# Kernel optimization log

Hardware: AMD Instinct MI355X
Metric: run time of the kernel (lower is better)

## Reference

```python
import jax, jax.numpy as jnp
import numpy as np

B, F, V, D = 4096, 24, 1000, 32
RED = 8            # max(1, F // 3) SENet bottleneck
COMB = 2 * F * D   # 1536
EPS = 1e-5


def setup_inputs() -> dict:
    key = jax.random.key(0)
    ks = jax.random.split(key, 12)
    return {
        "x": jax.random.randint(ks[0], (B, F), 0, V),
        "emb_tables": jax.random.normal(ks[1], (F, V, D), jnp.float32) * 0.05,
        "lin_tables": jax.random.normal(ks[2], (F, V), jnp.float32) * 0.05,
        "bias": jnp.zeros((1,), jnp.float32),
        "se_w1": jax.random.normal(ks[3], (RED, F), jnp.float32) * 0.2,
        "se_w2": jax.random.normal(ks[4], (F, RED), jnp.float32) * 0.2,
        "bil_W": jax.random.normal(ks[5], (F, F, D, D), jnp.float32) * (1.0 / np.sqrt(D)),
        "w0": jax.random.normal(ks[6], (COMB, 1024), jnp.float32) * 0.02,
        "b0": jnp.zeros((1024,), jnp.float32),
        "g0": jnp.ones((1024,), jnp.float32),
        "be0": jnp.zeros((1024,), jnp.float32),
        "w1": jax.random.normal(ks[7], (1024, 512), jnp.float32) * 0.02,
        "b1": jnp.zeros((512,), jnp.float32),
        "g1": jnp.ones((512,), jnp.float32),
        "be1": jnp.zeros((512,), jnp.float32),
        "w2": jax.random.normal(ks[8], (512, 1), jnp.float32) * 0.02,
        "b2": jnp.zeros((1,), jnp.float32),
    }


def _bilinear_field_interaction(e, W):
    # e: [B,F,D], W: [F,F,D,D]
    # out[b,i,k] = e[b,i,k] * sum_{j != i} (W[i,j] @ e[b,j])[k]
    t = jnp.einsum('ijkl,bjl->bijk', W, e)          # [B,F,F,D]
    mask = 1.0 - jnp.eye(F, dtype=e.dtype)          # zero the i==j terms
    s = jnp.einsum('bijk,ij->bik', t, mask)         # [B,F,D]
    return e * s


def _senet(e, w1, w2):
    Z = e.mean(axis=2)                              # [B,F] squeeze
    A = jax.nn.sigmoid(jax.nn.relu(Z @ w1.T) @ w2.T)  # [B,F]
    return e * A[:, :, None]


def _bn_train(h, g, b):
    m = h.mean(axis=0)
    v = h.var(axis=0)  # biased, matches torch BN normalization
    return g * (h - m) * jax.lax.rsqrt(v + EPS) + b


def reference(x, emb_tables, lin_tables, bias, se_w1, se_w2, bil_W,
              w0, b0, g0, be0, w1, b1, g1, be1, w2, b2):
    fidx = jnp.arange(F)[None, :]                   # [1,F]
    emb = emb_tables[fidx, x]                       # [B,F,D]
    lin = lin_tables[fidx, x].sum(axis=1)           # [B] first-order term

    se_emb = _senet(emb, se_w1, se_w2)
    p = _bilinear_field_interaction(emb, bil_W)     # [B,F,D]
    q = _bilinear_field_interaction(se_emb, bil_W)  # [B,F,D]
    combined = jnp.concatenate(
        [p.reshape(B, F * D), q.reshape(B, F * D)], axis=1)  # [B,2FD]

    h = jax.nn.relu(_bn_train(combined @ w0 + b0, g0, be0))
    h = jax.nn.relu(_bn_train(h @ w1 + b1, g1, be1))
    mlp_out = (h @ w2 + b2)[:, 0]                   # [B]

    logit = lin + bias[0] + mlp_out
    return jax.nn.sigmoid(logit)                    # [B]
```

## Files before the change

kernel.cpp:

```cpp
#include <hip/hip_runtime.h>

#define B_SZ 4096
#define F_SZ 24
#define V_SZ 1000
#define D_SZ 32
#define RED  8
#define FD   768
#define COMB 1536
#define H0   1024
#define H1   512
#define EPS  1e-5f

typedef __bf16 bf16x8 __attribute__((ext_vector_type(8)));
typedef float  f32x4  __attribute__((ext_vector_type(4)));
typedef const __attribute__((address_space(1))) unsigned int* gptr_t;
typedef       __attribute__((address_space(3))) unsigned int* lptr_t;

__device__ __forceinline__ float bf2f(unsigned short u) {
    union { unsigned int i; float f; } v; v.i = ((unsigned int)u) << 16; return v.f;
}
__device__ __forceinline__ unsigned short f2bf(float f) {
    union { float f; unsigned int i; } v; v.f = f;
    unsigned int u = v.i;
    return (unsigned short)((u + 0x7FFFu + ((u >> 16) & 1u)) >> 16);
}
__device__ __forceinline__ unsigned int pack2(float a, float b) {
    return (unsigned int)f2bf(a) | ((unsigned int)f2bf(b) << 16);
}

__global__ __launch_bounds__(256) void prep_gather(
        const int* __restrict__ x, const float* __restrict__ emb,
        const float* __restrict__ lint, const float* __restrict__ sw1,
        const float* __restrict__ sw2, const float* __restrict__ bw,
        const float* __restrict__ w0, const float* __restrict__ w1,
        unsigned short* __restrict__ Xbf, unsigned short* __restrict__ Wt,
        unsigned short* __restrict__ w0t, unsigned short* __restrict__ w1t,
        float* __restrict__ lin, float* __restrict__ sums) {
    int bid = blockIdx.x;
    int tid = threadIdx.x;
    if (bid < 1024) {
        int w = tid >> 6, lane = tid & 63;
        int b = bid * 4 + w;
        __shared__ int   xi[4][F_SZ];
        __shared__ float e[4][F_SZ][D_SZ];
        __shared__ float Z[4][F_SZ];
        __shared__ float r1[4][RED];
        __shared__ float Afac[4][F_SZ];
        if (lane < F_SZ) xi[w][lane] = x[b * F_SZ + lane];
        __syncthreads();
        #pragma unroll
        for (int it = 0; it < 3; it++) {
            int idx = it * 64 + lane;
            int f = idx >> 3, k4 = (idx & 7) * 4;
            float4 v = *(const float4*)&emb[((size_t)f * V_SZ + xi[w][f]) * D_SZ + k4];
            *(float4*)&e[w][f][k4] = v;
        }
        __syncthreads();
        if (lane < F_SZ) {
            float s = 0.f;
            #pragma unroll
            for (int k = 0; k < D_SZ; k++) s += e[w][lane][k];
            Z[w][lane] = s * (1.f / D_SZ);
        }
        __syncthreads();
        if (lane < RED) {
            float s = 0.f;
            #pragma unroll
            for (int f = 0; f < F_SZ; f++) s += Z[w][f] * sw1[lane * F_SZ + f];
            r1[w][lane] = fmaxf(s, 0.f);
        }
        __syncthreads();
        if (lane < F_SZ) {
            float s = 0.f;
            #pragma unroll
            for (int r = 0; r < RED; r++) s += r1[w][r] * sw2[lane * RED + r];
            Afac[w][lane] = 1.f / (1.f + expf(-s));
        }
        __syncthreads();
        #pragma unroll
        for (int it = 0; it < 3; it++) {
            int idx = it * 64 + lane;
            int f = idx >> 3, k4 = (idx & 7) * 4;
            const float* p = &e[w][f][k4];
            uint2 u, us;
            u.x = pack2(p[0], p[1]); u.y = pack2(p[2], p[3]);
            float a = Afac[w][f];
            us.x = pack2(p[0] * a, p[1] * a); us.y = pack2(p[2] * a, p[3] * a);
            *(uint2*)&Xbf[(size_t)b * FD + idx * 4] = u;
            *(uint2*)&Xbf[(size_t)(B_SZ + b) * FD + idx * 4] = us;
        }
        float lv = (lane < F_SZ) ? lint[lane * V_SZ + xi[w][lane]] : 0.f;
        #pragma unroll
        for (int off = 32; off > 0; off >>= 1) lv += __shfl_down(lv, off);
        if (lane == 0) lin[b] = lv;
    } else if (bid < 3328) {
        int o = (bid - 1024) * 256 + tid;
        int ik = o / FD, jl = o - ik * FD;
        int i = ik >> 5, k = ik & 31, j = jl >> 5, l = jl & 31;
        Wt[o] = (i == j) ? (unsigned short)0
                         : f2bf(bw[(((size_t)i * F_SZ + j) * D_SZ + k) * D_SZ + l]);
    } else if (bid < 5376) {
        __shared__ float tile[32][33];
        const float* in; unsigned short* out; int K, N, bx, by;
        if (bid < 4864) { int t = bid - 3328; in = w0; out = w0t; K = COMB; N = H0; bx = t & 31; by = t >> 5; }
        else            { int t = bid - 4864; in = w1; out = w1t; K = H0;   N = H1; bx = t & 15; by = t >> 4; }
        int tx = tid & 31, ty = tid >> 5;
        int n0 = bx * 32, k0 = by * 32;
        #pragma unroll
        for (int r = 0; r < 32; r += 8)
            tile[ty + r][tx] = in[(size_t)(k0 + ty + r) * N + n0 + tx];
        __syncthreads();
        #pragma unroll
        for (int r = 0; r < 32; r += 8)
            out[(size_t)(n0 + ty + r) * K + k0 + tx] = f2bf(tile[tx][ty + r]);
    } else {
        int o = (bid - 5376) * 256 + tid;
        sums[o] = 0.f;
    }
}

template<int MODE, int K, int N, int TM, int TN, int GX, int GY>
__global__ __launch_bounds__(256) void mfma_gemm(
        const unsigned short* __restrict__ A,
        const unsigned short* __restrict__ Bt,
        const float* __restrict__ bias,
        const unsigned short* __restrict__ Xbf,
        unsigned short* __restrict__ Obf,
        float* __restrict__ sum, float* __restrict__ sumsq,
        const float* __restrict__ psum, const float* __restrict__ psumsq,
        const float* __restrict__ g, const float* __restrict__ be) {
    constexpr int MI = TM / 32, NI = TN / 32;
    __shared__ unsigned short Abuf[TM * 32];
    __shared__ unsigned short Bbuf[TN * 32];
    __shared__ float sc_s[MODE == 2 ? K : 1];
    __shared__ float sh_s[MODE == 2 ? K : 1];
    const int tid  = threadIdx.x;
    const int lane = tid & 63, wv = tid >> 6;
    const int wm = (wv >> 1) * (TM / 2), wn = (wv & 1) * (TN / 2);
    const int fr = lane & 15, kq = lane >> 4;
    const int bid = blockIdx.x;
    const int xcd = bid & 7, slot = bid >> 3;
    const int rowb = xcd * (GY / 8) + slot / GX;
    const int colb = slot % GX;
    const int bm = rowb * TM, bn = colb * TN;
    const int srow = tid >> 2;
    const int skc  = (tid & 3) * 8;

    if (MODE == 2) {
        #pragma unroll
        for (int q = 0; q < K / 256; q++) {
            int c = q * 256 + tid;
            float m = psum[c] * (1.f / B_SZ);
            float var = psumsq[c] * (1.f / B_SZ) - m * m;
            float rstd = rsqrtf(var + EPS);
            float sc = g[c] * rstd;
            sc_s[c] = sc;
            sh_s[c] = be[c] - m * sc;
        }
        __syncthreads();
    }

    f32x4 acc[MI][NI];
    #pragma unroll
    for (int i = 0; i < MI; i++)
        #pragma unroll
        for (int j = 0; j < NI; j++) {
            f32x4 z = {0.f, 0.f, 0.f, 0.f};
            acc[i][j] = z;
        }

    for (int k0 = 0; k0 < K; k0 += 32) {
        if (MODE == 2) {
            uint4 hv = *(const uint4*)&A[(size_t)(bm + srow) * K + k0 + skc];
            unsigned int uu[4] = {hv.x, hv.y, hv.z, hv.w};
            unsigned int oo[4];
            #pragma unroll
            for (int q = 0; q < 4; q++) {
                int c = k0 + skc + 2 * q;
                float v0 = bf2f((unsigned short)(uu[q] & 0xFFFF)) * sc_s[c] + sh_s[c];
                float v1 = bf2f((unsigned short)(uu[q] >> 16)) * sc_s[c + 1] + sh_s[c + 1];
                oo[q] = pack2(fmaxf(v0, 0.f), fmaxf(v1, 0.f));
            }
            uint4 ov; ov.x = oo[0]; ov.y = oo[1]; ov.z = oo[2]; ov.w = oo[3];
            *(uint4*)&Abuf[srow * 32 + skc] = ov;
        } else {
            #pragma unroll
            for (int c = 0; c < TM / 64; c++) {
                const unsigned short* ga = A + (size_t)(bm + c * 64 + srow) * K + k0 + skc;
                char* la = (char*)Abuf + c * 4096 + wv * 1024;
                __builtin_amdgcn_global_load_lds((gptr_t)ga, (lptr_t)la, 16, 0, 0);
            }
        }
        #pragma unroll
        for (int c = 0; c < TN / 64; c++) {
            const unsigned short* gb = Bt + (size_t)(bn + c * 64 + srow) * K + k0 + skc;
            char* lb = (char*)Bbuf + c * 4096 + wv * 1024;
            __builtin_amdgcn_global_load_lds((gptr_t)gb, (lptr_t)lb, 16, 0, 0);
        }
        __syncthreads();
        bf16x8 af[MI], bfv[NI];
        #pragma unroll
        for (int mi = 0; mi < MI; mi++)
            af[mi] = *(const bf16x8*)&Abuf[(wm + mi * 16 + fr) * 32 + kq * 8];
        #pragma unroll
        for (int ni = 0; ni < NI; ni++)
            bfv[ni] = *(const bf16x8*)&Bbuf[(wn + ni * 16 + fr) * 32 + kq * 8];
        #pragma unroll
        for (int mi = 0; mi < MI; mi++)
            #pragma unroll
            for (int ni = 0; ni < NI; ni++)
                acc[mi][ni] = __builtin_amdgcn_mfma_f32_16x16x32_bf16(
                    af[mi], bfv[ni], acc[mi][ni], 0, 0, 0);
        __syncthreads();
    }

    if (MODE == 0) {
        #pragma unroll
        for (int mi = 0; mi < MI; mi++)
            #pragma unroll
            for (int ni = 0; ni < NI; ni++) {
                int col = bn + wn + ni * 16 + fr;
                #pragma unroll
                for (int r = 0; r < 4; r++) {
                    int row = bm + wm + mi * 16 + kq * 4 + r;
                    float xv = bf2f(Xbf[(size_t)row * FD + col]);
                    float cv = xv * acc[mi][ni][r];
                    size_t off = (row < B_SZ)
                        ? ((size_t)row * COMB + col)
                        : ((size_t)(row - B_SZ) * COMB + FD + col);
                    Obf[off] = f2bf(cv);
                }
            }
    } else {
        #pragma unroll
        for (int ni = 0; ni < NI; ni++) {
            int col = bn + wn + ni * 16 + fr;
            float bv = bias[col];
            float s = 0.f, ss = 0.f;
            #pragma unroll
            for (int mi = 0; mi < MI; mi++)
                #pragma unroll
                for (int r = 0; r < 4; r++) {
                    int row = bm + wm + mi * 16 + kq * 4 + r;
                    float v = acc[mi][ni][r] + bv;
                    Obf[(size_t)row * N + col] = f2bf(v);
                    s += v; ss += v * v;
                }
            s  += __shfl_xor(s, 16);  s  += __shfl_xor(s, 32);
            ss += __shfl_xor(ss, 16); ss += __shfl_xor(ss, 32);
            if (kq == 0) {
                atomicAdd(&sum[col], s);
                atomicAdd(&sumsq[col], ss);
            }
        }
    }
}

__global__ __launch_bounds__(256) void final_k(const unsigned short* __restrict__ h1,
        const float* __restrict__ sum, const float* __restrict__ sumsq,
        const float* __restrict__ g, const float* __restrict__ be,
        const float* __restrict__ w2, const float* __restrict__ b2,
        const float* __restrict__ lin, const float* __restrict__ bias,
        float* __restrict__ out) {
    __shared__ float sc_s[H1], sh_s[H1], w2_s[H1];
    int t = threadIdx.x;
    int wv = t >> 6, lane = t & 63;
    #pragma unroll
    for (int q = 0; q < 2; q++) {
        int c = q * 256 + t;
        float m = sum[c] * (1.f / B_SZ);
        float var = sumsq[c] * (1.f / B_SZ) - m * m;
        float rstd = rsqrtf(var + EPS);
        float sc = g[c] * rstd;
        sc_s[c] = sc;
        sh_s[c] = be[c] - m * sc;
        w2_s[c] = w2[c];
    }
    __syncthreads();
    int r0 = blockIdx.x * 16;
    #pragma unroll
    for (int i = 0; i < 4; i++) {
        int row = r0 + wv * 4 + i;
        int c0 = lane * 8;
        uint4 hv = *(const uint4*)&h1[(size_t)row * H1 + c0];
        unsigned int uu[4] = {hv.x, hv.y, hv.z, hv.w};
        float acc = 0.f;
        #pragma unroll
        for (int q = 0; q < 4; q++) {
            int c = c0 + 2 * q;
            float v0 = bf2f((unsigned short)(uu[q] & 0xFFFF)) * sc_s[c] + sh_s[c];
            float v1 = bf2f((unsigned short)(uu[q] >> 16)) * sc_s[c + 1] + sh_s[c + 1];
            acc += fmaxf(v0, 0.f) * w2_s[c] + fmaxf(v1, 0.f) * w2_s[c + 1];
        }
        #pragma unroll
        for (int off = 32; off > 0; off >>= 1) acc += __shfl_down(acc, off);
        if (lane == 0) {
            float logit = lin[row] + bias[0] + acc + b2[0];
            out[row] = 1.f / (1.f + expf(-logit));
        }
    }
}

extern "C" void kernel_launch(void* const* d_in, const int* in_sizes, int n_in,
                              void* d_out, int out_size, void* d_ws, size_t ws_size,
                              hipStream_t stream) {
    const int*   x    = (const int*)d_in[0];
    const float* emb  = (const float*)d_in[1];
    const float* lint = (const float*)d_in[2];
    const float* bias = (const float*)d_in[3];
    const float* sw1  = (const float*)d_in[4];
    const float* sw2  = (const float*)d_in[5];
    const float* bw   = (const float*)d_in[6];
    const float* w0   = (const float*)d_in[7];
    const float* b0   = (const float*)d_in[8];
    const float* g0   = (const float*)d_in[9];
    const float* be0  = (const float*)d_in[10];
    const float* w1   = (const float*)d_in[11];
    const float* b1   = (const float*)d_in[12];
    const float* g1   = (const float*)d_in[13];
    const float* be1  = (const float*)d_in[14];
    const float* w2   = (const float*)d_in[15];
    const float* b2   = (const float*)d_in[16];
    float* out = (float*)d_out;

    char* p = (char*)d_ws;
    auto alloc = [&](size_t bytes) { char* r = p; p += (bytes + 255) & ~(size_t)255; return r; };

    unsigned short* Xbf  = (unsigned short*)alloc((size_t)2 * B_SZ * FD * 2);
    unsigned short* Wt   = (unsigned short*)alloc((size_t)FD * FD * 2);
    unsigned short* w0t  = (unsigned short*)alloc((size_t)H0 * COMB * 2);
    unsigned short* w1t  = (unsigned short*)alloc((size_t)H1 * H0 * 2);
    unsigned short* Cbf  = (unsigned short*)alloc((size_t)B_SZ * COMB * 2);
    unsigned short* h0bf = (unsigned short*)alloc((size_t)B_SZ * H0 * 2);
    unsigned short* h1bf = (unsigned short*)alloc((size_t)B_SZ * H1 * 2);
    float* lin = (float*)alloc(B_SZ * 4);
    float* sums = (float*)alloc((2 * H0 + 2 * H1) * 4);
    float* sum0 = sums, *sumsq0 = sums + H0, *sum1 = sums + 2 * H0, *sumsq1 = sums + 2 * H0 + H1;

    prep_gather<<<5388, 256, 0, stream>>>(x, emb, lint, sw1, sw2, bw, w0, w1,
                                          Xbf, Wt, w0t, w1t, lin, sums);

    mfma_gemm<0, FD, FD, 128, 64, 12, 64><<<768, 256, 0, stream>>>(
        Xbf, Wt, nullptr, Xbf, Cbf, nullptr, nullptr, nullptr, nullptr, nullptr, nullptr);
    mfma_gemm<1, COMB, H0, 128, 64, 16, 32><<<512, 256, 0, stream>>>(
        Cbf, w0t, b0, nullptr, h0bf, sum0, sumsq0, nullptr, nullptr, nullptr, nullptr);
    mfma_gemm<2, H0, H1, 64, 64, 8, 64><<<512, 256, 0, stream>>>(
        h0bf, w1t, b1, nullptr, h1bf, sum1, sumsq1, sum0, sumsq0, g0, be0);
    final_k<<<B_SZ / 16, 256, 0, stream>>>(h1bf, sum1, sumsq1, g1, be1,
                                           w2, b2, lin, bias, out);
}
```

Before: 177.3 us.

## Double K-step per barrier and stage GEMM epilogue through LDS for vector stores

The MFMA GEMM main loop now loads two 32-wide K slices per iteration, which halves the number of __syncthreads barriers. In the BN-fused mode it also prefetches the next A slice into registers before the MFMAs run. The epilogue writes the accumulators into a padded LDS tile and then emits 16-byte bf16 stores, with the X-multiply applied during that pass, instead of scattered 2-byte stores. The cost is more LDS use per block, which may lower occupancy. The store pass assumes a 64-column tile per 32-row pass.

```diff
diff --git a/kernel.cpp b/kernel.cpp
--- a/kernel.cpp
+++ b/kernel.cpp
@@ -130,8 +130,14 @@
         const float* __restrict__ psum, const float* __restrict__ psumsq,
         const float* __restrict__ g, const float* __restrict__ be) {
     constexpr int MI = TM / 32, NI = TN / 32;
-    __shared__ unsigned short Abuf[TM * 32];
-    __shared__ unsigned short Bbuf[TN * 32];
+    constexpr int CLD = TN + 4;
+    constexpr int STAGE = (TM + TN) * 128;
+    constexpr int CST   = TM * CLD * 4;
+    constexpr int SMEM  = STAGE > CST ? STAGE : CST;
+    __shared__ __align__(16) char smem[SMEM];
+    unsigned short* Abuf = (unsigned short*)smem;
+    unsigned short* Bbuf = (unsigned short*)(smem + TM * 128);
+    float* Cst = (float*)smem;
     __shared__ float sc_s[MODE == 2 ? K : 1];
     __shared__ float sh_s[MODE == 2 ? K : 1];
     const int tid  = threadIdx.x;
@@ -169,69 +175,73 @@
             acc[i][j] = z;
         }
 
-    for (int k0 = 0; k0 < K; k0 += 32) {
+    uint4 hvA[2];
+    if (MODE == 2) {
+        #pragma unroll
+        for (int s = 0; s < 2; s++)
+            hvA[s] = *(const uint4*)&A[(size_t)(bm + srow) * K + 32 * s + skc];
+    }
+
+    for (int k0 = 0; k0 < K; k0 += 64) {
         if (MODE == 2) {
-            uint4 hv = *(const uint4*)&A[(size_t)(bm + srow) * K + k0 + skc];
-            unsigned int uu[4] = {hv.x, hv.y, hv.z, hv.w};
-            unsigned int oo[4];
-            #pragma unroll
-            for (int q = 0; q < 4; q++) {
-                int c = k0 + skc + 2 * q;
-                float v0 = bf2f((unsigned short)(uu[q] & 0xFFFF)) * sc_s[c] + sh_s[c];
-                float v1 = bf2f((unsigned short)(uu[q] >> 16)) * sc_s[c + 1] + sh_s[c + 1];
-                oo[q] = pack2(fmaxf(v0, 0.f), fmaxf(v1, 0.f));
+            #pragma unroll
+            for (int s = 0; s < 2; s++) {
+                unsigned int uu[4] = {hvA[s].x, hvA[s].y, hvA[s].z, hvA[s].w};
+                unsigned int oo[4];
+                #pragma unroll
+                for (int q = 0; q < 4; q++) {
+                    int c = k0 + 32 * s + skc + 2 * q;
+                    float v0 = bf2f((unsigned short)(uu[q] & 0xFFFF)) * sc_s[c] + sh_s[c];
+                    float v1 = bf2f((unsigned short)(uu[q] >> 16)) * sc_s[c + 1] + sh_s[c + 1];
+                    oo[q] = pack2(fmaxf(v0, 0.f), fmaxf(v1, 0.f));
+                }
+                uint4 ov; ov.x = oo[0]; ov.y = oo[1]; ov.z = oo[2]; ov.w = oo[3];
+                *(uint4*)&Abuf[s * TM * 32 + srow * 32 + skc] = ov;
             }
-            uint4 ov; ov.x = oo[0]; ov.y = oo[1]; ov.z = oo[2]; ov.w = oo[3];
-            *(uint4*)&Abuf[srow * 32 + skc] = ov;
+            if (k0 + 64 < K) {
+                #pragma unroll
+                for (int s = 0; s < 2; s++)
+                    hvA[s] = *(const uint4*)&A[(size_t)(bm + srow) * K + k0 + 64 + 32 * s + skc];
+            }
         } else {
             #pragma unroll
-            for (int c = 0; c < TM / 64; c++) {
-                const unsigned short* ga = A + (size_t)(bm + c * 64 + srow) * K + k0 + skc;
-                char* la = (char*)Abuf + c * 4096 + wv * 1024;
-                __builtin_amdgcn_global_load_lds((gptr_t)ga, (lptr_t)la, 16, 0, 0);
+            for (int s = 0; s < 2; s++)
+                #pragma unroll
+                for (int c = 0; c < TM / 64; c++) {
+                    const unsigned short* ga = A + (size_t)(bm + c * 64 + srow) * K + k0 + 32 * s + skc;
+                    char* la = smem + s * TM * 64 + c * 4096 + wv * 1024;
+                    __builtin_amdgcn_global_load_lds((gptr_t)ga, (lptr_t)la, 16, 0, 0);
+                }
+        }
+        #pragma unroll
+        for (int s = 0; s < 2; s++)
+            #pragma unroll
+            for (int c = 0; c < TN / 64; c++) {
+                const unsigned short* gb = Bt + (size_t)(bn + c * 64 + srow) * K + k0 + 32 * s + skc;
+                char* lb = smem + TM * 128 + s * TN * 64 + c * 4096 + wv * 1024;
+                __builtin_amdgcn_global_load_lds((gptr_t)gb, (lptr_t)lb, 16, 0, 0);
             }
-        }
-        #pragma unroll
-        for (int c = 0; c < TN / 64; c++) {
-            const unsigned short* gb = Bt + (size_t)(bn + c * 64 + srow) * K + k0 + skc;
-            char* lb = (char*)Bbuf + c * 4096 + wv * 1024;
-            __builtin_amdgcn_global_load_lds((gptr_t)gb, (lptr_t)lb, 16, 0, 0);
-        }
-        __syncthreads();
-        bf16x8 af[MI], bfv[NI];
-        #pragma unroll
-        for (int mi = 0; mi < MI; mi++)
-            af[mi] = *(const bf16x8*)&Abuf[(wm + mi * 16 + fr) * 32 + kq * 8];
-        #pragma unroll
-        for (int ni = 0; ni < NI; ni++)
-            bfv[ni] = *(const bf16x8*)&Bbuf[(wn + ni * 16 + fr) * 32 + kq * 8];
-        #pragma unroll
-        for (int mi = 0; mi < MI; mi++)
+        __syncthreads();
+        #pragma unroll
+        for (int s = 0; s < 2; s++) {
+            bf16x8 af[MI], bfv[NI];
+            #pragma unroll
+            for (int mi = 0; mi < MI; mi++)
+                af[mi] = *(const bf16x8*)&Abuf[s * TM * 32 + (wm + mi * 16 + fr) * 32 + kq * 8];
             #pragma unroll
             for (int ni = 0; ni < NI; ni++)
-                acc[mi][ni] = __builtin_amdgcn_mfma_f32_16x16x32_bf16(
-                    af[mi], bfv[ni], acc[mi][ni], 0, 0, 0);
-        __syncthreads();
-    }
-
-    if (MODE == 0) {
-        #pragma unroll
-        for (int mi = 0; mi < MI; mi++)
-            #pragma unroll
-            for (int ni = 0; ni < NI; ni++) {
-                int col = bn + wn + ni * 16 + fr;
+                bfv[ni] = *(const bf16x8*)&Bbuf[s * TN * 32 + (wn + ni * 16 + fr) * 32 + kq * 8];
+            #pragma unroll
+            for (int mi = 0; mi < MI; mi++)
                 #pragma unroll
-                for (int r = 0; r < 4; r++) {
-                    int row = bm + wm + mi * 16 + kq * 4 + r;
-                    float xv = bf2f(Xbf[(size_t)row * FD + col]);
-                    float cv = xv * acc[mi][ni][r];
-                    size_t off = (row < B_SZ)
-                        ? ((size_t)row * COMB + col)
-                        : ((size_t)(row - B_SZ) * COMB + FD + col);
-                    Obf[off] = f2bf(cv);
-                }
-            }
-    } else {
+                for (int ni = 0; ni < NI; ni++)
+                    acc[mi][ni] = __builtin_amdgcn_mfma_f32_16x16x32_bf16(
+                        af[mi], bfv[ni], acc[mi][ni], 0, 0, 0);
+        }
+        __syncthreads();
+    }
+
+    if (MODE != 0) {
         #pragma unroll
         for (int ni = 0; ni < NI; ni++) {
             int col = bn + wn + ni * 16 + fr;
@@ -241,9 +251,8 @@
             for (int mi = 0; mi < MI; mi++)
                 #pragma unroll
                 for (int r = 0; r < 4; r++) {
-                    int row = bm + wm + mi * 16 + kq * 4 + r;
                     float v = acc[mi][ni][r] + bv;
-                    Obf[(size_t)row * N + col] = f2bf(v);
+                    acc[mi][ni][r] = v;
                     s += v; ss += v * v;
                 }
             s  += __shfl_xor(s, 16);  s  += __shfl_xor(s, 32);
@@ -252,6 +261,50 @@
                 atomicAdd(&sum[col], s);
                 atomicAdd(&sumsq[col], ss);
             }
+        }
+    }
+
+    #pragma unroll
+    for (int mi = 0; mi < MI; mi++)
+        #pragma unroll
+        for (int ni = 0; ni < NI; ni++) {
+            int lrow = wm + mi * 16 + kq * 4;
+            int lcol = wn + ni * 16 + fr;
+            #pragma unroll
+            for (int r = 0; r < 4; r++)
+                Cst[(lrow + r) * CLD + lcol] = acc[mi][ni][r];
+        }
+    __syncthreads();
+    #pragma unroll
+    for (int ps = 0; ps < TM / 32; ps++) {
+        int rl = ps * 32 + (tid >> 3);
+        int cl = (tid & 7) * 8;
+        float4 va = *(const float4*)&Cst[rl * CLD + cl];
+        float4 vb = *(const float4*)&Cst[rl * CLD + cl + 4];
+        float v[8] = {va.x, va.y, va.z, va.w, vb.x, vb.y, vb.z, vb.w};
+        int grow = bm + rl, gcol = bn + cl;
+        if (MODE == 0) {
+            uint4 xv = *(const uint4*)&Xbf[(size_t)grow * FD + gcol];
+            unsigned int xu[4] = {xv.x, xv.y, xv.z, xv.w};
+            unsigned int oo[4];
+            #pragma unroll
+            for (int q = 0; q < 4; q++) {
+                float x0 = bf2f((unsigned short)(xu[q] & 0xFFFF));
+                float x1 = bf2f((unsigned short)(xu[q] >> 16));
+                oo[q] = pack2(x0 * v[2 * q], x1 * v[2 * q + 1]);
+            }
+            uint4 ov; ov.x = oo[0]; ov.y = oo[1]; ov.z = oo[2]; ov.w = oo[3];
+            size_t off = (grow < B_SZ)
+                ? ((size_t)grow * COMB + gcol)
+                : ((size_t)(grow - B_SZ) * COMB + FD + gcol);
+            *(uint4*)&Obf[off] = ov;
+        } else {
+            unsigned int oo[4];
+            #pragma unroll
+            for (int q = 0; q < 4; q++)
+                oo[q] = pack2(v[2 * q], v[2 * q + 1]);
+            uint4 ov; ov.x = oo[0]; ov.y = oo[1]; ov.z = oo[2]; ov.w = oo[3];
+            *(uint4*)&Obf[(size_t)grow * N + gcol] = ov;
         }
     }
 }
```

Result: faster. 165.8 us (-6.5%).
